# Optimization experiments

Measured on AMD Instinct MI355X. Metric: run time of the kernel, lower is better.

Reference implementation:

```python
import jax, jax.numpy as jnp
import numpy as np

G = 8          # group (window) size -> N = G*G = 64
HEADS = 8
DIM = 256
HEAD_DIM = DIM // HEADS
SCALE = HEAD_DIM ** -0.5
POS_DIM = (DIM // 4) // 4  # 16
LN_EPS = 1e-5


def _make_bias_tables():
    # biases: coordinates (1-g..g-1) x (1-g..g-1) -> [(2g-1)^2, 2] float
    r = np.arange(1 - G, G)
    bh, bw = np.meshgrid(r, r, indexing='ij')
    biases = np.stack([bh.ravel(), bw.ravel()], axis=1).astype(np.float32)
    # relative position index [g^2, g^2]
    ch, cw = np.meshgrid(np.arange(G), np.arange(G), indexing='ij')
    coords = np.stack([ch.ravel(), cw.ravel()])              # [2, g^2]
    rel = coords[:, :, None] - coords[:, None, :]            # [2, g^2, g^2]
    rel = rel.transpose(1, 2, 0)
    rel[:, :, 0] += G - 1
    rel[:, :, 1] += G - 1
    rel[:, :, 0] *= 2 * G - 1
    rel_idx = rel.sum(-1).astype(np.int32)                   # [g^2, g^2]
    return biases, rel_idx


def setup_inputs() -> dict:
    key = jax.random.key(0)
    ks = jax.random.split(key, 8)
    B, N, C = 2048, G * G, DIM
    biases_np, rel_idx_np = _make_bias_tables()
    s = lambda fan: 1.0 / np.sqrt(fan)
    return {
        'x': jax.random.normal(ks[0], (B, N, C), jnp.float32),
        'qkv_w': jax.random.normal(ks[1], (C, 3 * C), jnp.float32) * s(C),
        'qkv_b': jnp.zeros((3 * C,), jnp.float32),
        'proj_w': jax.random.normal(ks[2], (C, C), jnp.float32) * s(C),
        'proj_b': jnp.zeros((C,), jnp.float32),
        'pos_proj_w': jax.random.normal(ks[3], (2, POS_DIM), jnp.float32) * s(2),
        'pos_proj_b': jnp.zeros((POS_DIM,), jnp.float32),
        'ln1_g': jnp.ones((POS_DIM,), jnp.float32), 'ln1_b': jnp.zeros((POS_DIM,), jnp.float32),
        'fc1_w': jax.random.normal(ks[4], (POS_DIM, POS_DIM), jnp.float32) * s(POS_DIM),
        'fc1_b': jnp.zeros((POS_DIM,), jnp.float32),
        'ln2_g': jnp.ones((POS_DIM,), jnp.float32), 'ln2_b': jnp.zeros((POS_DIM,), jnp.float32),
        'fc2_w': jax.random.normal(ks[5], (POS_DIM, POS_DIM), jnp.float32) * s(POS_DIM),
        'fc2_b': jnp.zeros((POS_DIM,), jnp.float32),
        'ln3_g': jnp.ones((POS_DIM,), jnp.float32), 'ln3_b': jnp.zeros((POS_DIM,), jnp.float32),
        'fc3_w': jax.random.normal(ks[6], (POS_DIM, HEADS), jnp.float32) * s(POS_DIM),
        'fc3_b': jnp.zeros((HEADS,), jnp.float32),
        'biases': jnp.asarray(biases_np),
        'rel_idx': jnp.asarray(rel_idx_np),
    }


def _ln(h, g, b):
    m = jnp.mean(h, -1, keepdims=True)
    v = jnp.mean((h - m) ** 2, -1, keepdims=True)
    return (h - m) * jax.lax.rsqrt(v + LN_EPS) * g + b


def reference(x, qkv_w, qkv_b, proj_w, proj_b,
              pos_proj_w, pos_proj_b,
              ln1_g, ln1_b, fc1_w, fc1_b,
              ln2_g, ln2_b, fc2_w, fc2_b,
              ln3_g, ln3_b, fc3_w, fc3_b,
              biases, rel_idx):
    B, N, C = x.shape
    # dynamic position bias MLP: [(2g-1)^2, 2] -> [(2g-1)^2, heads]
    h = biases @ pos_proj_w + pos_proj_b
    h = jax.nn.relu(_ln(h, ln1_g, ln1_b)) @ fc1_w + fc1_b
    h = jax.nn.relu(_ln(h, ln2_g, ln2_b)) @ fc2_w + fc2_b
    pos = jax.nn.relu(_ln(h, ln3_g, ln3_b)) @ fc3_w + fc3_b        # [225, H]
    rel_bias = pos[rel_idx]                                        # [N, N, H]
    rel_bias = jnp.transpose(rel_bias, (2, 0, 1))                  # [H, N, N]

    qkv = (x @ qkv_w + qkv_b).reshape(B, N, 3, HEADS, HEAD_DIM)
    qkv = jnp.transpose(qkv, (2, 0, 3, 1, 4))                      # [3, B, H, N, Dh]
    q, k, v = qkv[0] * SCALE, qkv[1], qkv[2]
    attn = jnp.einsum('bhnd,bhmd->bhnm', q, k) + rel_bias[None]    # [B, H, N, N]
    attn = jax.nn.softmax(attn, axis=-1)
    out = jnp.einsum('bhnm,bhmd->bhnd', attn, v)                   # [B, H, N, Dh]
    out = jnp.transpose(out, (0, 2, 1, 3)).reshape(B, N, C)
    return out @ proj_w + proj_b
```

## Files before the change

### kernel.cpp

```cpp
#include <hip/hip_runtime.h>

typedef _Float16 half_t;
typedef __attribute__((ext_vector_type(8))) _Float16 half8;
typedef __attribute__((ext_vector_type(4))) _Float16 half4;
typedef __attribute__((ext_vector_type(4))) float float4v;

#define LN_EPS 1e-5f
#define QK_SCALE 0.17677669529663687f

static __device__ __forceinline__ float4v mfma_16x16x32(half8 a, half8 b, float4v c) {
    return __builtin_amdgcn_mfma_f32_16x16x32_f16(a, b, c, 0, 0, 0);
}

static __device__ __forceinline__ int swz512(int row, int colByte) {
    return row * 512 + ((((colByte >> 4) ^ (row & 7)) << 4) | (colByte & 15));
}
static __device__ __forceinline__ int swz128(int row, int colByte) {
    return row * 128 + ((((colByte >> 4) ^ (row & 7)) << 4) | (colByte & 15));
}

static __device__ void ln_relu16(float* h, const float* __restrict__ g, const float* __restrict__ b) {
    float m = 0.f;
    for (int j = 0; j < 16; ++j) m += h[j];
    m *= (1.0f / 16.0f);
    float v = 0.f;
    for (int j = 0; j < 16; ++j) { float d = h[j] - m; v += d * d; }
    v *= (1.0f / 16.0f);
    float rs = rsqrtf(v + LN_EPS);
    for (int j = 0; j < 16; ++j) {
        float t = (h[j] - m) * rs * g[j] + b[j];
        h[j] = t > 0.f ? t : 0.f;
    }
}

__global__ void prep_kernel(
    const float* __restrict__ qkv_w,
    const float* __restrict__ proj_w,
    const float* __restrict__ biases,
    const float* __restrict__ pos_w, const float* __restrict__ pos_b,
    const float* __restrict__ ln1_g, const float* __restrict__ ln1_b,
    const float* __restrict__ fc1_w, const float* __restrict__ fc1_b,
    const float* __restrict__ ln2_g, const float* __restrict__ ln2_b,
    const float* __restrict__ fc2_w, const float* __restrict__ fc2_b,
    const float* __restrict__ ln3_g, const float* __restrict__ ln3_b,
    const float* __restrict__ fc3_w, const float* __restrict__ fc3_b,
    const int* __restrict__ rel_idx,
    half_t* __restrict__ wqkvT,
    half_t* __restrict__ wprojT,
    float* __restrict__ rel_bias)
{
    __shared__ float tile[64][65];
    __shared__ float pos_s[225][8];
    const int t = blockIdx.x;
    const int tid = threadIdx.x;

    if (t < 64) {
        const float* src; half_t* dst; int ncols, rg, cg;
        if (t < 48) { src = qkv_w;  dst = wqkvT;  ncols = 768; rg = t / 12;      cg = t % 12; }
        else        { src = proj_w; dst = wprojT; ncols = 256; rg = (t-48) >> 2; cg = (t-48) & 3; }
        const int r0 = tid >> 6, c = tid & 63;
        for (int i = 0; i < 16; ++i) {
            int r = i * 4 + r0;
            tile[r][c] = src[(rg * 64 + r) * ncols + cg * 64 + c];
        }
        __syncthreads();
        for (int i = 0; i < 16; ++i) {
            int r = i * 4 + r0;
            dst[(cg * 64 + r) * 256 + rg * 64 + c] = (half_t)tile[c][r];
        }
    } else {
        if (tid < 225) {
            float h[16], h2[16];
            float b0 = biases[tid * 2], b1 = biases[tid * 2 + 1];
            for (int j = 0; j < 16; ++j) h[j] = b0 * pos_w[j] + b1 * pos_w[16 + j] + pos_b[j];
            ln_relu16(h, ln1_g, ln1_b);
            for (int j = 0; j < 16; ++j) {
                float s = fc1_b[j];
                for (int k = 0; k < 16; ++k) s += h[k] * fc1_w[k * 16 + j];
                h2[j] = s;
            }
            ln_relu16(h2, ln2_g, ln2_b);
            for (int j = 0; j < 16; ++j) {
                float s = fc2_b[j];
                for (int k = 0; k < 16; ++k) s += h2[k] * fc2_w[k * 16 + j];
                h[j] = s;
            }
            ln_relu16(h, ln3_g, ln3_b);
            for (int j = 0; j < 8; ++j) {
                float s = fc3_b[j];
                for (int k = 0; k < 16; ++k) s += h[k] * fc3_w[k * 8 + j];
                pos_s[tid][j] = s;
            }
        }
        __syncthreads();
        for (int e = tid; e < 8 * 64 * 64; e += 256) {
            int hh = e >> 12, nm = e & 4095;
            rel_bias[e] = pos_s[rel_idx[nm]][hh];
        }
    }
}

__global__ __launch_bounds__(512, 2) void fused_kernel(
    const float* __restrict__ x,
    const half_t* __restrict__ wqkvT,
    const float* __restrict__ qkv_b,
    const half_t* __restrict__ wprojT,
    const float* __restrict__ proj_b,
    const float* __restrict__ rel_bias,
    float* __restrict__ out)
{
    __shared__ __align__(16) char smem[131072];
    char* xs = smem;
    char* qs = smem + 32768;
    char* ks = smem + 65536;
    char* vt = smem + 98304;

    const int b   = blockIdx.x;
    const int tid = threadIdx.x;
    const int w   = tid >> 6;
    const int lane = tid & 63;
    const int m = lane & 15;
    const int g = lane >> 4;

    const float* xg = x + (size_t)b * (64 * 256);
    #pragma unroll
    for (int i = 0; i < 8; ++i) {
        int u = tid + i * 512;
        int row = u >> 6, c4 = u & 63;
        float4v xv = *(const float4v*)(xg + u * 4);
        half4 hv;
        hv[0] = (half_t)xv[0]; hv[1] = (half_t)xv[1];
        hv[2] = (half_t)xv[2]; hv[3] = (half_t)xv[3];
        *(half4*)(xs + swz512(row, c4 * 8)) = hv;
    }
    __syncthreads();

    for (int ct6 = 0; ct6 < 6; ++ct6) {
        const int ct = w * 6 + ct6;
        half8 bfr[8];
        const half_t* wb = wqkvT + (ct * 16 + m) * 256 + g * 8;
        #pragma unroll
        for (int kk = 0; kk < 8; ++kk) bfr[kk] = *(const half8*)(wb + kk * 32);
        const float bias = qkv_b[ct * 16 + m];
        #pragma unroll
        for (int ti = 0; ti < 4; ++ti) {
            float4v acc = {0.f, 0.f, 0.f, 0.f};
            #pragma unroll
            for (int kk = 0; kk < 8; ++kk) {
                half8 af = *(const half8*)(xs + swz512(ti * 16 + m, kk * 64 + g * 16));
                acc = mfma_16x16x32(af, bfr[kk], acc);
            }
            if (ct < 16) {
                int colB = (ct * 16 + m) * 2;
                #pragma unroll
                for (int r = 0; r < 4; ++r)
                    *(half_t*)(qs + swz512(ti * 16 + g * 4 + r, colB)) = (half_t)(acc[r] + bias);
            } else if (ct < 32) {
                int colB = ((ct - 16) * 16 + m) * 2;
                #pragma unroll
                for (int r = 0; r < 4; ++r)
                    *(half_t*)(ks + swz512(ti * 16 + g * 4 + r, colB)) = (half_t)(acc[r] + bias);
            } else {
                int d = (ct - 32) * 16 + m;
                half4 pv;
                #pragma unroll
                for (int r = 0; r < 4; ++r) pv[r] = (half_t)(acc[r] + bias);
                *(half4*)(vt + swz128(d, (ti * 16 + g * 4) * 2)) = pv;
            }
        }
    }
    __syncthreads();

    const int h = w;
    half8 bk[4];
    #pragma unroll
    for (int tj = 0; tj < 4; ++tj)
        bk[tj] = *(const half8*)(ks + swz512(tj * 16 + m, h * 64 + g * 16));
    float4v sacc[4][4];
    #pragma unroll
    for (int ti = 0; ti < 4; ++ti) {
        half8 aq = *(const half8*)(qs + swz512(ti * 16 + m, h * 64 + g * 16));
        #pragma unroll
        for (int tj = 0; tj < 4; ++tj) {
            float4v z = {0.f, 0.f, 0.f, 0.f};
            sacc[ti][tj] = mfma_16x16x32(aq, bk[tj], z);
        }
    }
    __syncthreads();

    const float* rb = rel_bias + h * 4096;
    char* pw = smem + w * 8192;
    float rinv[4][4];
    #pragma unroll
    for (int ti = 0; ti < 4; ++ti) {
        #pragma unroll
        for (int r = 0; r < 4; ++r) {
            int row = ti * 16 + g * 4 + r;
            float v0 = sacc[ti][0][r] * QK_SCALE + rb[row * 64 + m];
            float v1 = sacc[ti][1][r] * QK_SCALE + rb[row * 64 + 16 + m];
            float v2 = sacc[ti][2][r] * QK_SCALE + rb[row * 64 + 32 + m];
            float v3 = sacc[ti][3][r] * QK_SCALE + rb[row * 64 + 48 + m];
            float mx = fmaxf(fmaxf(v0, v1), fmaxf(v2, v3));
            mx = fmaxf(mx, __shfl_xor(mx, 1));
            mx = fmaxf(mx, __shfl_xor(mx, 2));
            mx = fmaxf(mx, __shfl_xor(mx, 4));
            mx = fmaxf(mx, __shfl_xor(mx, 8));
            float e0 = __expf(v0 - mx), e1 = __expf(v1 - mx);
            float e2 = __expf(v2 - mx), e3 = __expf(v3 - mx);
            float s = e0 + e1 + e2 + e3;
            s += __shfl_xor(s, 1); s += __shfl_xor(s, 2);
            s += __shfl_xor(s, 4); s += __shfl_xor(s, 8);
            rinv[ti][r] = 1.0f / s;
            *(half_t*)(pw + swz128(row, 2 * m))      = (half_t)e0;
            *(half_t*)(pw + swz128(row, 2 * m + 32)) = (half_t)e1;
            *(half_t*)(pw + swz128(row, 2 * m + 64)) = (half_t)e2;
            *(half_t*)(pw + swz128(row, 2 * m + 96)) = (half_t)e3;
        }
    }

    half8 bv[2][2];
    #pragma unroll
    for (int tjd = 0; tjd < 2; ++tjd)
        #pragma unroll
        for (int kk = 0; kk < 2; ++kk)
            bv[tjd][kk] = *(const half8*)(vt + swz128(h * 32 + tjd * 16 + m, kk * 64 + g * 16));
    #pragma unroll
    for (int ti = 0; ti < 4; ++ti) {
        half8 pa0 = *(const half8*)(pw + swz128(ti * 16 + m, g * 16));
        half8 pa1 = *(const half8*)(pw + swz128(ti * 16 + m, 64 + g * 16));
        #pragma unroll
        for (int tjd = 0; tjd < 2; ++tjd) {
            float4v o = {0.f, 0.f, 0.f, 0.f};
            o = mfma_16x16x32(pa0, bv[tjd][0], o);
            o = mfma_16x16x32(pa1, bv[tjd][1], o);
            #pragma unroll
            for (int r = 0; r < 4; ++r) {
                float val = o[r] * rinv[ti][r];
                *(half_t*)(ks + swz512(ti * 16 + g * 4 + r, (h * 32 + tjd * 16 + m) * 2)) = (half_t)val;
            }
        }
    }
    __syncthreads();

    float* og = out + (size_t)b * (64 * 256);
    #pragma unroll
    for (int cti = 0; cti < 2; ++cti) {
        const int ct = w * 2 + cti;
        half8 bf[8];
        const half_t* wb = wprojT + (ct * 16 + m) * 256 + g * 8;
        #pragma unroll
        for (int kk = 0; kk < 8; ++kk) bf[kk] = *(const half8*)(wb + kk * 32);
        const float pb = proj_b[ct * 16 + m];
        #pragma unroll
        for (int ti = 0; ti < 4; ++ti) {
            float4v acc = {0.f, 0.f, 0.f, 0.f};
            #pragma unroll
            for (int kk = 0; kk < 8; ++kk) {
                half8 af = *(const half8*)(ks + swz512(ti * 16 + m, kk * 64 + g * 16));
                acc = mfma_16x16x32(af, bf[kk], acc);
            }
            #pragma unroll
            for (int r = 0; r < 4; ++r)
                og[(ti * 16 + g * 4 + r) * 256 + ct * 16 + m] = acc[r] + pb;
        }
    }
}

extern "C" void kernel_launch(void* const* d_in, const int* in_sizes, int n_in,
                              void* d_out, int out_size, void* d_ws, size_t ws_size,
                              hipStream_t stream) {
    const float* x          = (const float*)d_in[0];
    const float* qkv_w      = (const float*)d_in[1];
    const float* qkv_b      = (const float*)d_in[2];
    const float* proj_w     = (const float*)d_in[3];
    const float* proj_b     = (const float*)d_in[4];
    const float* pos_proj_w = (const float*)d_in[5];
    const float* pos_proj_b = (const float*)d_in[6];
    const float* ln1_g = (const float*)d_in[7];
    const float* ln1_b = (const float*)d_in[8];
    const float* fc1_w = (const float*)d_in[9];
    const float* fc1_b = (const float*)d_in[10];
    const float* ln2_g = (const float*)d_in[11];
    const float* ln2_b = (const float*)d_in[12];
    const float* fc2_w = (const float*)d_in[13];
    const float* fc2_b = (const float*)d_in[14];
    const float* ln3_g = (const float*)d_in[15];
    const float* ln3_b = (const float*)d_in[16];
    const float* fc3_w = (const float*)d_in[17];
    const float* fc3_b = (const float*)d_in[18];
    const float* biases = (const float*)d_in[19];
    const int*  rel_idx = (const int*)d_in[20];

    half_t* wqkvT    = (half_t*)d_ws;
    half_t* wprojT   = (half_t*)((char*)d_ws + 393216);
    float*  rel_bias = (float*)((char*)d_ws + 524288);

    const int B = in_sizes[0] / (64 * 256);

    prep_kernel<<<65, 256, 0, stream>>>(qkv_w, proj_w, biases, pos_proj_w, pos_proj_b,
                                        ln1_g, ln1_b, fc1_w, fc1_b,
                                        ln2_g, ln2_b, fc2_w, fc2_b,
                                        ln3_g, ln3_b, fc3_w, fc3_b,
                                        rel_idx, wqkvT, wprojT, rel_bias);
    fused_kernel<<<B, 512, 0, stream>>>(x, wqkvT, qkv_b, wprojT, proj_b, rel_bias,
                                        (float*)d_out);
}
```

Baseline: 270.9 us.

## Keep per-head Q/K/V in registers and shrink LDS to raise occupancy

Each wave now computes its own head's Q, K and V projections directly, rather than having waves split the QKV columns and exchange the results through shared memory. The fragments are reshuffled through a small per-wave scratch area, so the large Q/K/V LDS buffers and several block-wide barriers go away. LDS drops from 128KB to 80KB and launch bounds go from 2 to 4 blocks per SM. The relative-position bias is pre-permuted so each lane reads it as a float4, and the QKV/proj GEMMs now process two column tiles per pass to reuse A-fragments. The higher register pressure may cause spills at the new occupancy target.

```diff
diff --git a/kernel.cpp b/kernel.cpp
--- a/kernel.cpp
+++ b/kernel.cpp
@@ -8,15 +8,15 @@
 #define LN_EPS 1e-5f
 #define QK_SCALE 0.17677669529663687f
 
-static __device__ __forceinline__ float4v mfma_16x16x32(half8 a, half8 b, float4v c) {
+static __device__ __forceinline__ float4v mfma16(half8 a, half8 b, float4v c) {
     return __builtin_amdgcn_mfma_f32_16x16x32_f16(a, b, c, 0, 0, 0);
 }
 
-static __device__ __forceinline__ int swz512(int row, int colByte) {
-    return row * 512 + ((((colByte >> 4) ^ (row & 7)) << 4) | (colByte & 15));
-}
-static __device__ __forceinline__ int swz128(int row, int colByte) {
-    return row * 128 + ((((colByte >> 4) ^ (row & 7)) << 4) | (colByte & 15));
+static __device__ __forceinline__ int swzA(int row, int colByte) {
+    return row * 512 + ((((colByte >> 4) ^ ((row >> 1) & 7)) << 4) | (colByte & 15));
+}
+static __device__ __forceinline__ int swzB(int row, int colByte) {
+    return row * 64 + ((((colByte >> 4) ^ ((row >> 1) & 3)) << 4) | (colByte & 15));
 }
 
 static __device__ void ln_relu16(float* h, const float* __restrict__ g, const float* __restrict__ b) {
@@ -47,7 +47,7 @@
     const int* __restrict__ rel_idx,
     half_t* __restrict__ wqkvT,
     half_t* __restrict__ wprojT,
-    float* __restrict__ rel_bias)
+    float* __restrict__ rbp)
 {
     __shared__ float tile[64][65];
     __shared__ float pos_s[225][8];
@@ -94,35 +94,38 @@
         }
         __syncthreads();
         for (int e = tid; e < 8 * 64 * 64; e += 256) {
-            int hh = e >> 12, nm = e & 4095;
-            rel_bias[e] = pos_s[rel_idx[nm]][hh];
-        }
-    }
-}
-
-__global__ __launch_bounds__(512, 2) void fused_kernel(
+            int hh = e >> 12, rem = e & 4095;
+            int row = rem >> 6, c = rem & 63;
+            int tj = c >> 4, mm = c & 15;
+            rbp[hh * 4096 + row * 64 + mm * 4 + tj] = pos_s[rel_idx[row * 64 + c]][hh];
+        }
+    }
+}
+
+__global__ __launch_bounds__(512, 4) void fused_kernel(
     const float* __restrict__ x,
     const half_t* __restrict__ wqkvT,
     const float* __restrict__ qkv_b,
     const half_t* __restrict__ wprojT,
     const float* __restrict__ proj_b,
-    const float* __restrict__ rel_bias,
+    const float* __restrict__ rbp,
     float* __restrict__ out)
 {
-    __shared__ __align__(16) char smem[131072];
-    char* xs = smem;
-    char* qs = smem + 32768;
-    char* ks = smem + 65536;
-    char* vt = smem + 98304;
+    __shared__ __align__(16) char smem[81920];
+    char* xs  = smem;
+    char* atn = smem + 32768;
+    char* scr = smem + 65536;
 
     const int b   = blockIdx.x;
     const int tid = threadIdx.x;
-    const int w   = tid >> 6;
+    const int w    = tid >> 6;
     const int lane = tid & 63;
     const int m = lane & 15;
     const int g = lane >> 4;
-
-    const float* xg = x + (size_t)b * (64 * 256);
+    char* wscr   = scr + w * 2048;
+    char* parena = xs  + w * 4096;
+
+    const float* xg = x + (size_t)b * 16384;
     #pragma unroll
     for (int i = 0; i < 8; ++i) {
         int u = tid + i * 512;
@@ -131,75 +134,68 @@
         half4 hv;
         hv[0] = (half_t)xv[0]; hv[1] = (half_t)xv[1];
         hv[2] = (half_t)xv[2]; hv[3] = (half_t)xv[3];
-        *(half4*)(xs + swz512(row, c4 * 8)) = hv;
+        *(half4*)(xs + swzA(row, c4 * 8)) = hv;
     }
     __syncthreads();
 
-    for (int ct6 = 0; ct6 < 6; ++ct6) {
-        const int ct = w * 6 + ct6;
-        half8 bfr[8];
-        const half_t* wb = wqkvT + (ct * 16 + m) * 256 + g * 8;
-        #pragma unroll
-        for (int kk = 0; kk < 8; ++kk) bfr[kk] = *(const half8*)(wb + kk * 32);
-        const float bias = qkv_b[ct * 16 + m];
-        #pragma unroll
-        for (int ti = 0; ti < 4; ++ti) {
-            float4v acc = {0.f, 0.f, 0.f, 0.f};
-            #pragma unroll
-            for (int kk = 0; kk < 8; ++kk) {
-                half8 af = *(const half8*)(xs + swz512(ti * 16 + m, kk * 64 + g * 16));
-                acc = mfma_16x16x32(af, bfr[kk], acc);
-            }
-            if (ct < 16) {
-                int colB = (ct * 16 + m) * 2;
+    half8 aq[4], bk[4];
+    #pragma unroll
+    for (int pt = 0; pt < 2; ++pt) {
+        const int wrow0 = pt * 256 + w * 32;
+        float4v acc[2][4];
+        #pragma unroll
+        for (int c2 = 0; c2 < 2; ++c2)
+            #pragma unroll
+            for (int ti = 0; ti < 4; ++ti) acc[c2][ti] = {0.f, 0.f, 0.f, 0.f};
+        #pragma unroll
+        for (int kk = 0; kk < 8; ++kk) {
+            half8 wf0 = *(const half8*)(wqkvT + (size_t)(wrow0 +      m) * 256 + kk * 32 + g * 8);
+            half8 wf1 = *(const half8*)(wqkvT + (size_t)(wrow0 + 16 + m) * 256 + kk * 32 + g * 8);
+            #pragma unroll
+            for (int ti = 0; ti < 4; ++ti) {
+                half8 af = *(const half8*)(xs + swzA(ti * 16 + m, kk * 64 + g * 16));
+                acc[0][ti] = mfma16(wf0, af, acc[0][ti]);
+                acc[1][ti] = mfma16(wf1, af, acc[1][ti]);
+            }
+        }
+        half4 pk[2][4];
+        #pragma unroll
+        for (int c2 = 0; c2 < 2; ++c2) {
+            #pragma unroll
+            for (int ti = 0; ti < 4; ++ti)
                 #pragma unroll
                 for (int r = 0; r < 4; ++r)
-                    *(half_t*)(qs + swz512(ti * 16 + g * 4 + r, colB)) = (half_t)(acc[r] + bias);
-            } else if (ct < 32) {
-                int colB = ((ct - 16) * 16 + m) * 2;
-                #pragma unroll
-                for (int r = 0; r < 4; ++r)
-                    *(half_t*)(ks + swz512(ti * 16 + g * 4 + r, colB)) = (half_t)(acc[r] + bias);
-            } else {
-                int d = (ct - 32) * 16 + m;
-                half4 pv;
-                #pragma unroll
-                for (int r = 0; r < 4; ++r) pv[r] = (half_t)(acc[r] + bias);
-                *(half4*)(vt + swz128(d, (ti * 16 + g * 4) * 2)) = pv;
-            }
-        }
-    }
-    __syncthreads();
-
-    const int h = w;
-    half8 bk[4];
-    #pragma unroll
-    for (int tj = 0; tj < 4; ++tj)
-        bk[tj] = *(const half8*)(ks + swz512(tj * 16 + m, h * 64 + g * 16));
-    float4v sacc[4][4];
+                    pk[c2][ti][r] = (half_t)(acc[c2][ti][r] + qkv_b[wrow0 + c2 * 16 + g * 4 + r]);
+        }
+        #pragma unroll
+        for (int ti = 0; ti < 4; ++ti) {
+            *(half4*)(wscr + swzB(m, (g * 4) * 2))        = pk[0][ti];
+            *(half4*)(wscr + swzB(m, (16 + g * 4) * 2))   = pk[1][ti];
+            half8 fr = *(const half8*)(wscr + swzB(m, g * 16));
+            if (pt == 0) aq[ti] = fr; else bk[ti] = fr;
+        }
+    }
+
+    float rinv[4][4];
+    half4 ph[4][4];
+    const float* rbh = rbp + w * 4096;
     #pragma unroll
     for (int ti = 0; ti < 4; ++ti) {
-        half8 aq = *(const half8*)(qs + swz512(ti * 16 + m, h * 64 + g * 16));
-        #pragma unroll
-        for (int tj = 0; tj < 4; ++tj) {
-            float4v z = {0.f, 0.f, 0.f, 0.f};
-            sacc[ti][tj] = mfma_16x16x32(aq, bk[tj], z);
-        }
-    }
-    __syncthreads();
-
-    const float* rb = rel_bias + h * 4096;
-    char* pw = smem + w * 8192;
-    float rinv[4][4];
-    #pragma unroll
-    for (int ti = 0; ti < 4; ++ti) {
+        float4v z = {0.f, 0.f, 0.f, 0.f};
+        float4v s0 = mfma16(aq[ti], bk[0], z);
+        float4v s1 = mfma16(aq[ti], bk[1], z);
+        float4v s2 = mfma16(aq[ti], bk[2], z);
+        float4v s3 = mfma16(aq[ti], bk[3], z);
+        float4v rb[4];
+        #pragma unroll
+        for (int r = 0; r < 4; ++r)
+            rb[r] = *(const float4v*)(rbh + (ti * 16 + g * 4 + r) * 64 + m * 4);
         #pragma unroll
         for (int r = 0; r < 4; ++r) {
-            int row = ti * 16 + g * 4 + r;
-            float v0 = sacc[ti][0][r] * QK_SCALE + rb[row * 64 + m];
-            float v1 = sacc[ti][1][r] * QK_SCALE + rb[row * 64 + 16 + m];
-            float v2 = sacc[ti][2][r] * QK_SCALE + rb[row * 64 + 32 + m];
-            float v3 = sacc[ti][3][r] * QK_SCALE + rb[row * 64 + 48 + m];
+            float v0 = s0[r] * QK_SCALE + rb[r][0];
+            float v1 = s1[r] * QK_SCALE + rb[r][1];
+            float v2 = s2[r] * QK_SCALE + rb[r][2];
+            float v3 = s3[r] * QK_SCALE + rb[r][3];
             float mx = fmaxf(fmaxf(v0, v1), fmaxf(v2, v3));
             mx = fmaxf(mx, __shfl_xor(mx, 1));
             mx = fmaxf(mx, __shfl_xor(mx, 2));
@@ -211,59 +207,110 @@
             s += __shfl_xor(s, 1); s += __shfl_xor(s, 2);
             s += __shfl_xor(s, 4); s += __shfl_xor(s, 8);
             rinv[ti][r] = 1.0f / s;
-            *(half_t*)(pw + swz128(row, 2 * m))      = (half_t)e0;
-            *(half_t*)(pw + swz128(row, 2 * m + 32)) = (half_t)e1;
-            *(half_t*)(pw + swz128(row, 2 * m + 64)) = (half_t)e2;
-            *(half_t*)(pw + swz128(row, 2 * m + 96)) = (half_t)e3;
-        }
-    }
-
-    half8 bv[2][2];
+            ph[ti][0][r] = (half_t)e0;
+            ph[ti][1][r] = (half_t)e1;
+            ph[ti][2][r] = (half_t)e2;
+            ph[ti][3][r] = (half_t)e3;
+        }
+    }
+
+    half4 vh[2][4];
+    {
+        const int wrow0 = 512 + w * 32;
+        float4v acc[2][4];
+        #pragma unroll
+        for (int c2 = 0; c2 < 2; ++c2)
+            #pragma unroll
+            for (int ti = 0; ti < 4; ++ti) acc[c2][ti] = {0.f, 0.f, 0.f, 0.f};
+        #pragma unroll
+        for (int kk = 0; kk < 8; ++kk) {
+            half8 wf0 = *(const half8*)(wqkvT + (size_t)(wrow0 +      m) * 256 + kk * 32 + g * 8);
+            half8 wf1 = *(const half8*)(wqkvT + (size_t)(wrow0 + 16 + m) * 256 + kk * 32 + g * 8);
+            #pragma unroll
+            for (int ti = 0; ti < 4; ++ti) {
+                half8 af = *(const half8*)(xs + swzA(ti * 16 + m, kk * 64 + g * 16));
+                acc[0][ti] = mfma16(af, wf0, acc[0][ti]);
+                acc[1][ti] = mfma16(af, wf1, acc[1][ti]);
+            }
+        }
+        float vb0 = qkv_b[wrow0 + m], vb1 = qkv_b[wrow0 + 16 + m];
+        #pragma unroll
+        for (int c2 = 0; c2 < 2; ++c2)
+            #pragma unroll
+            for (int ti = 0; ti < 4; ++ti)
+                #pragma unroll
+                for (int r = 0; r < 4; ++r)
+                    vh[c2][ti][r] = (half_t)(acc[c2][ti][r] + (c2 ? vb1 : vb0));
+    }
+    __syncthreads();
+
+    float4v oacc[2][4];
     #pragma unroll
     for (int tjd = 0; tjd < 2; ++tjd)
         #pragma unroll
-        for (int kk = 0; kk < 2; ++kk)
-            bv[tjd][kk] = *(const half8*)(vt + swz128(h * 32 + tjd * 16 + m, kk * 64 + g * 16));
-    #pragma unroll
-    for (int ti = 0; ti < 4; ++ti) {
-        half8 pa0 = *(const half8*)(pw + swz128(ti * 16 + m, g * 16));
-        half8 pa1 = *(const half8*)(pw + swz128(ti * 16 + m, 64 + g * 16));
-        #pragma unroll
-        for (int tjd = 0; tjd < 2; ++tjd) {
-            float4v o = {0.f, 0.f, 0.f, 0.f};
-            o = mfma_16x16x32(pa0, bv[tjd][0], o);
-            o = mfma_16x16x32(pa1, bv[tjd][1], o);
+        for (int ti = 0; ti < 4; ++ti) oacc[tjd][ti] = {0.f, 0.f, 0.f, 0.f};
+    #pragma unroll
+    for (int nc = 0; nc < 2; ++nc) {
+        #pragma unroll
+        for (int ti = 0; ti < 4; ++ti)
+            #pragma unroll
+            for (int t2 = 0; t2 < 2; ++t2)
+                #pragma unroll
+                for (int r = 0; r < 4; ++r)
+                    *(half_t*)(parena + swzB(ti * 16 + g * 4 + r, (t2 * 16 + m) * 2)) =
+                        ph[ti][nc * 2 + t2][r];
+        #pragma unroll
+        for (int c2 = 0; c2 < 2; ++c2)
+            #pragma unroll
+            for (int t2 = 0; t2 < 2; ++t2)
+                *(half4*)(wscr + swzB(c2 * 16 + m, (t2 * 16 + g * 4) * 2)) = vh[c2][nc * 2 + t2];
+        half8 bv0 = *(const half8*)(wscr + swzB(m, g * 16));
+        half8 bv1 = *(const half8*)(wscr + swzB(16 + m, g * 16));
+        #pragma unroll
+        for (int ti = 0; ti < 4; ++ti) {
+            half8 pa = *(const half8*)(parena + swzB(ti * 16 + m, g * 16));
+            oacc[0][ti] = mfma16(pa, bv0, oacc[0][ti]);
+            oacc[1][ti] = mfma16(pa, bv1, oacc[1][ti]);
+        }
+    }
+    #pragma unroll
+    for (int tjd = 0; tjd < 2; ++tjd)
+        #pragma unroll
+        for (int ti = 0; ti < 4; ++ti)
             #pragma unroll
             for (int r = 0; r < 4; ++r) {
-                float val = o[r] * rinv[ti][r];
-                *(half_t*)(ks + swz512(ti * 16 + g * 4 + r, (h * 32 + tjd * 16 + m) * 2)) = (half_t)val;
-            }
-        }
-    }
+                float val = oacc[tjd][ti][r] * rinv[ti][r];
+                *(half_t*)(atn + swzA(ti * 16 + g * 4 + r, (w * 32 + tjd * 16 + m) * 2)) = (half_t)val;
+            }
     __syncthreads();
 
-    float* og = out + (size_t)b * (64 * 256);
-    #pragma unroll
-    for (int cti = 0; cti < 2; ++cti) {
-        const int ct = w * 2 + cti;
-        half8 bf[8];
-        const half_t* wb = wprojT + (ct * 16 + m) * 256 + g * 8;
-        #pragma unroll
-        for (int kk = 0; kk < 8; ++kk) bf[kk] = *(const half8*)(wb + kk * 32);
-        const float pb = proj_b[ct * 16 + m];
+    float* og = out + (size_t)b * 16384;
+    const int oc0 = w * 32;
+    float4v pacc[2][4];
+    #pragma unroll
+    for (int c2 = 0; c2 < 2; ++c2)
+        #pragma unroll
+        for (int ti = 0; ti < 4; ++ti) pacc[c2][ti] = {0.f, 0.f, 0.f, 0.f};
+    #pragma unroll
+    for (int kk = 0; kk < 8; ++kk) {
+        half8 wf0 = *(const half8*)(wprojT + (size_t)(oc0 +      m) * 256 + kk * 32 + g * 8);
+        half8 wf1 = *(const half8*)(wprojT + (size_t)(oc0 + 16 + m) * 256 + kk * 32 + g * 8);
         #pragma unroll
         for (int ti = 0; ti < 4; ++ti) {
-            float4v acc = {0.f, 0.f, 0.f, 0.f};
-            #pragma unroll
-            for (int kk = 0; kk < 8; ++kk) {
-                half8 af = *(const half8*)(ks + swz512(ti * 16 + m, kk * 64 + g * 16));
-                acc = mfma_16x16x32(af, bf[kk], acc);
-            }
+            half8 af = *(const half8*)(atn + swzA(ti * 16 + m, kk * 64 + g * 16));
+            pacc[0][ti] = mfma16(af, wf0, pacc[0][ti]);
+            pacc[1][ti] = mfma16(af, wf1, pacc[1][ti]);
+        }
+    }
+    float pb0 = proj_b[oc0 + m], pb1 = proj_b[oc0 + 16 + m];
+    #pragma unroll
+    for (int c2 = 0; c2 < 2; ++c2)
+        #pragma unroll
+        for (int ti = 0; ti < 4; ++ti)
             #pragma unroll
             for (int r = 0; r < 4; ++r)
-                og[(ti * 16 + g * 4 + r) * 256 + ct * 16 + m] = acc[r] + pb;
-        }
-    }
+                og[(ti * 16 + g * 4 + r) * 256 + oc0 + c2 * 16 + m] =
+                    pacc[c2][ti][r] + (c2 ? pb1 : pb0);
 }
 
 extern "C" void kernel_launch(void* const* d_in, const int* in_sizes, int n_in,
@@ -291,9 +338,9 @@
     const float* biases = (const float*)d_in[19];
     const int*  rel_idx = (const int*)d_in[20];
 
-    half_t* wqkvT    = (half_t*)d_ws;
-    half_t* wprojT   = (half_t*)((char*)d_ws + 393216);
-    float*  rel_bias = (float*)((char*)d_ws + 524288);
+    half_t* wqkvT  = (half_t*)d_ws;
+    half_t* wprojT = (half_t*)((char*)d_ws + 393216);
+    float*  rbp    = (float*)((char*)d_ws + 524288);
 
     const int B = in_sizes[0] / (64 * 256);
 
@@ -301,7 +348,7 @@
                                         ln1_g, ln1_b, fc1_w, fc1_b,
                                         ln2_g, ln2_b, fc2_w, fc2_b,
                                         ln3_g, ln3_b, fc3_w, fc3_b,
-                                        rel_idx, wqkvT, wprojT, rel_bias);
-    fused_kernel<<<B, 512, 0, stream>>>(x, wqkvT, qkv_b, wprojT, proj_b, rel_bias,
+                                        rel_idx, wqkvT, wprojT, rbp);
+    fused_kernel<<<B, 512, 0, stream>>>(x, wqkvT, qkv_b, wprojT, proj_b, rbp,
                                         (float*)d_out);
 }
```

New measurement: 340.0 us. 25.5% more time.
